# Kernel tuning notes

Hardware: AMD Instinct MI355X
Metric: run time of the kernel (lower is better)

Reference implementation:

```python
import jax, jax.numpy as jnp
import numpy as np

NUM_HEADS = 12
TOP_R = 0.1


def attention_rollout(attn_stack):
    # attn_stack: [L, B, H, N1, N1]; head_fusion='mean'
    A = attn_stack.mean(axis=2)                       # [L, B, N1, N1]
    n1 = A.shape[-1]
    A = A + jnp.eye(n1, dtype=A.dtype)                # residual connection
    A = A / A.sum(axis=-1, keepdims=True)             # row-normalize
    rollout = A[0]
    for l in range(1, A.shape[0]):                    # small fixed loop over layers
        rollout = A[l] @ rollout
    return rollout                                    # [B, N1, N1]


def setup_inputs() -> dict:
    key = jax.random.key(0)
    ks = jax.random.split(key, 7)
    B, N1, D, L, H = 32, 197, 768, 12, NUM_HEADS
    s = 1.0 / np.sqrt(D)
    return {
        "x": jax.random.normal(ks[0], (B, N1, D), dtype=jnp.float32),
        "attn_stack": jax.random.uniform(ks[1], (L, B, H, N1, N1), dtype=jnp.float32),
        "q_w": jax.random.normal(ks[2], (D, D), dtype=jnp.float32) * s,
        "k_w": jax.random.normal(ks[3], (D, D), dtype=jnp.float32) * s,
        "v_w": jax.random.normal(ks[4], (D, D), dtype=jnp.float32) * s,
        "proj_w": jax.random.normal(ks[5], (D, D), dtype=jnp.float32) * s,
        "proj_b": jnp.zeros((D,), dtype=jnp.float32),
    }


def reference(x, attn_stack, q_w, k_w, v_w, proj_w, proj_b):
    B, N1, C = x.shape
    N = N1 - 1
    H = NUM_HEADS
    hd = C // H
    scale = hd ** (-0.5)

    # --- attention rollout (detached in original) -> CLS attention over patches ---
    rollout = attention_rollout(jax.lax.stop_gradient(attn_stack))  # [B, N1, N1]
    cls_attention = rollout[:, 0, 1:]                               # [B, N]
    R = int(N * TOP_R)                                              # static top-R count
    _, top_indices = jax.lax.top_k(cls_attention, R)                # [B, R]

    # --- gather top-R local tokens (shift by 1 to skip CLS) ---
    x_local = jnp.take_along_axis(x, (top_indices + 1)[:, :, None], axis=1)  # [B, R, C]

    # --- projections ---
    q = (x_local @ q_w.T).reshape(B, R, H, hd).transpose(0, 2, 1, 3)   # [B, H, R, hd]
    k = (x @ k_w.T).reshape(B, N1, H, hd).transpose(0, 2, 1, 3)        # [B, H, N1, hd]
    v = (x @ v_w.T).reshape(B, N1, H, hd).transpose(0, 2, 1, 3)        # [B, H, N1, hd]

    # --- cross attention: local queries vs global key/values ---
    attn = jnp.einsum('bhrd,bhnd->bhrn', q, k) * scale                 # [B, H, R, N1]
    attn = jax.nn.softmax(attn, axis=-1)
    out = jnp.einsum('bhrn,bhnd->bhrd', attn, v)                       # [B, H, R, hd]
    out = out.transpose(0, 2, 1, 3).reshape(B, R, C)

    # --- output projection ---
    out = out @ proj_w.T + proj_b
    return out
```

## Files before the change

kernel.cpp:

```cpp
#include <hip/hip_runtime.h>
#include <math.h>

#define L_  12
#define B_  32
#define H_  12
#define N1_ 197
#define D_  768
#define R_  19
#define M_TOK (B_ * N1_)
#define NN (N1_ * N1_)

#define K1_FULL_ROWS  69344
#define K1_ROWS       69376
#define K1_BLOCKS     (K1_ROWS / 4)
#define PACK_ROWS     (M_TOK + 2304)
#define PACK_BLOCKS   ((PACK_ROWS * 12 + 255) / 256)
#define QKV_TILES     630

typedef __attribute__((ext_vector_type(8))) _Float16 f16x8;
typedef __attribute__((ext_vector_type(4))) float f32x4;

__device__ __forceinline__ f32x4 ld4u(const float* p) {
  f32x4 r; __builtin_memcpy(&r, p, 16); return r;
}
__device__ __forceinline__ void st4u(float* p, f32x4 v) {
  __builtin_memcpy(p, &v, 16);
}

__device__ __forceinline__ ushort f2h_bits(float f) {
  _Float16 h = (_Float16)f;
  ushort u; __builtin_memcpy(&u, &h, 2); return u;
}

typedef const __attribute__((address_space(1))) void* as1_vp;
typedef __attribute__((address_space(3))) void* as3_vp;
__device__ __forceinline__ void gl_lds16(const void* g, void* s) {
  __builtin_amdgcn_global_load_lds((as1_vp)g, (as3_vp)s, 16, 0, 0);
}

__global__ __launch_bounds__(256) void mega_k1_pack(const float* __restrict__ attn,
                                                    float* __restrict__ P,
                                                    float* __restrict__ dvec,
                                                    const float* __restrict__ x,
                                                    const float* __restrict__ k_w,
                                                    const float* __restrict__ v_w,
                                                    const float* __restrict__ q_w,
                                                    ushort* __restrict__ xpack,
                                                    ushort* __restrict__ wpack) {
  int bid = blockIdx.x;
  if (bid < K1_BLOCKS) {
    int wid = threadIdx.x >> 6;
    int t   = threadIdx.x & 63;
    int row_id = bid * 4 + wid;
    int l, b, i;
    if (row_id < K1_FULL_ROWS) {
      l = row_id / 6304;
      int rem = row_id - l * 6304;
      b = rem / 197;
      i = rem - b * 197;
    } else {
      l = 11; b = row_id - K1_FULL_ROWS; i = 0;
    }
    int lb   = l * B_ + b;
    int prow = lb * N1_ + i;
    const float* base = attn + (size_t)lb * (H_ * NN) + (size_t)i * N1_;
    f32x4 acc = {0.f, 0.f, 0.f, 0.f};
    if (t < 49) {
      const float* p = base + 4 * t;
#pragma unroll
      for (int h = 0; h < H_; ++h) acc += ld4u(p + (size_t)h * NN);
    } else if (t == 49) {
      const float* p = base + 196;
#pragma unroll
      for (int h = 0; h < H_; ++h) acc.x += p[(size_t)h * NN];
    }
    float s = (acc.x + acc.y) + (acc.z + acc.w);
#pragma unroll
    for (int o = 32; o; o >>= 1) s += __shfl_xor(s, o);
    float inv = 1.f / (s + 12.f);
    float* Pr = P + (size_t)prow * N1_;
    if (t < 49)       st4u(Pr + 4 * t, acc * inv);
    else if (t == 49) Pr[196] = acc.x * inv;
    if (t == 0) dvec[prow] = 12.f * inv;
  } else {
    int t = (bid - K1_BLOCKS) * 256 + threadIdx.x;
    if (t >= PACK_ROWS * 12) return;
    int row = t / 12, kb = t - row * 12;
    const float* src;
    ushort* dst;
    if (row < M_TOK) {
      src = x + (size_t)row * D_;
      dst = xpack + (size_t)row * 768;
    } else {
      int wr = row - M_TOK;
      int g = wr / 768, rl = wr - g * 768;
      const float* wsrc = (g == 0) ? k_w : (g == 1) ? v_w : q_w;
      src = wsrc + (size_t)rl * D_;
      dst = wpack + (size_t)wr * 768;
    }
    src += kb * 64;
    dst += kb * 64;
#pragma unroll
    for (int u = 0; u < 8; ++u) {
      float4 f = *(const float4*)(src + u * 8);
      float4 g = *(const float4*)(src + u * 8 + 4);
      f16x8 h;
      h[0] = (_Float16)f.x; h[1] = (_Float16)f.y;
      h[2] = (_Float16)f.z; h[3] = (_Float16)f.w;
      h[4] = (_Float16)g.x; h[5] = (_Float16)g.y;
      h[6] = (_Float16)g.z; h[7] = (_Float16)g.w;
      *(f16x8*)(dst + u * 8) = h;
    }
  }
}

__global__ __launch_bounds__(1024) void k2_chain_topk(const float* __restrict__ P,
                                                      const float* __restrict__ dvec,
                                                      int* __restrict__ gidx) {
  int b = blockIdx.x;
  __shared__ float v[N1_];
  __shared__ float part[4][N1_];
  int t = threadIdx.x, quar = t >> 8, j = t & 255;

  if (t < N1_) {
    const float* Pr = P + ((size_t)(11 * B_ + b) * N1_) * N1_;
    v[t] = Pr[t] + (t == 0 ? dvec[(11 * B_ + b) * N1_] : 0.f);
  }
  __syncthreads();

  for (int l = 10; l >= 0; --l) {
    if (j < N1_) {
      const float* Pc = P + ((size_t)(l * B_ + b) * N1_) * N1_ + j;
      float a[8] = {0.f, 0.f, 0.f, 0.f, 0.f, 0.f, 0.f, 0.f};
      int ibeg = (quar * N1_) / 4;
      int iend = ((quar + 1) * N1_) / 4;
      int i = ibeg;
      for (; i + 8 <= iend; i += 8) {
#pragma unroll
        for (int u = 0; u < 8; ++u)
          a[u] += v[i + u] * Pc[(size_t)(i + u) * N1_];
      }
      for (; i < iend; ++i) a[0] += v[i] * Pc[(size_t)i * N1_];
      float s = ((a[0] + a[1]) + (a[2] + a[3])) + ((a[4] + a[5]) + (a[6] + a[7]));
      if (quar == 0) s += v[j] * dvec[(l * B_ + b) * N1_ + j];
      part[quar][j] = s;
    }
    __syncthreads();
    if (t < N1_) v[t] = (part[0][t] + part[1][t]) + (part[2][t] + part[3][t]);
    __syncthreads();
  }

  if (t < 64) {
    float val[4];
    int   idx[4];
#pragma unroll
    for (int c = 0; c < 4; ++c) {
      int n = t + c * 64;
      bool ok = (n < N1_ - 1);
      val[c] = ok ? v[n + 1] : -1e30f;
      idx[c] = ok ? n : (1 << 20);
    }
    for (int r = 0; r < R_; ++r) {
      float bv = val[0];
      int   bi = idx[0];
#pragma unroll
      for (int c = 1; c < 4; ++c)
        if (val[c] > bv || (val[c] == bv && idx[c] < bi)) { bv = val[c]; bi = idx[c]; }
#pragma unroll
      for (int o = 32; o; o >>= 1) {
        float ov = __shfl_xor(bv, o);
        int   oi = __shfl_xor(bi, o);
        if (ov > bv || (ov == bv && oi < bi)) { bv = ov; bi = oi; }
      }
      if (t == 0) gidx[b * R_ + r] = b * N1_ + bi + 1;
#pragma unroll
      for (int c = 0; c < 4; ++c)
        if (idx[c] == bi) val[c] = -1e30f;
    }
  }
}

__global__ __launch_bounds__(256) void gemm_kvq_fast(const ushort* __restrict__ xpack,
                                                     const ushort* __restrict__ wpack,
                                                     const int* __restrict__ gidx,
                                                     float* __restrict__ kvb,
                                                     float* __restrict__ qbuf) {
  __shared__ __attribute__((aligned(16))) ushort As[128 * 64];
  __shared__ __attribute__((aligned(16))) ushort Bs[128 * 64];
  int tid = threadIdx.x, lane = tid & 63, wid = tid >> 6;
  int wr = wid >> 1, wc = wid & 1;
  int lr = lane & 15, lk = lane >> 4;

  int bid = blockIdx.x;
  int bm, wrow0, ccol0, ldc, Mrows;
  float* C;
  bool gath;
  if (bid < 600) {
    bm = bid % 50; int bn = bid / 50;
    wrow0 = bn * 128; ccol0 = bn * 128; ldc = 1536; Mrows = M_TOK;
    C = kvb; gath = false;
  } else {
    int tq = bid - 600;
    bm = tq % 5; int bn = tq / 5;
    wrow0 = 1536 + bn * 128; ccol0 = bn * 128; ldc = 768; Mrows = 608;
    C = qbuf; gath = true;
  }

  const ushort* asrc[4];
  const ushort* bsrc[4];
  ushort* adst[4];
  ushort* bdst[4];
  int lrow = lane >> 3, cpr = lane & 7;
#pragma unroll
  for (int i = 0; i < 4; ++i) {
    int r_loc = wid * 32 + i * 8 + lrow;
    int c     = cpr ^ (r_loc & 7);
    int ga    = bm * 128 + r_loc; if (ga >= Mrows) ga = Mrows - 1;
    int arow  = gath ? gidx[ga] : ga;
    asrc[i] = xpack + (size_t)arow * 768 + c * 8;
    bsrc[i] = wpack + (size_t)(wrow0 + r_loc) * 768 + c * 8;
    adst[i] = &As[(wid * 32 + i * 8) * 64];
    bdst[i] = &Bs[(wid * 32 + i * 8) * 64];
  }

  int o0 = (lk ^ (lr & 7)) * 8;
  int o1 = o0 ^ 32;

  f32x4 acc[4][4] = {};

#pragma unroll
  for (int i = 0; i < 4; ++i) { gl_lds16(asrc[i], adst[i]); gl_lds16(bsrc[i], bdst[i]); }

  for (int kb = 0; kb < 12; ++kb) {
    __syncthreads();
    f16x8 af0[4], af1[4], bf0[4], bf1[4];
#pragma unroll
    for (int m = 0; m < 4; ++m) {
      const ushort* rp = &As[(wr * 64 + m * 16 + lr) * 64];
      af0[m] = *(const f16x8*)(rp + o0);
      af1[m] = *(const f16x8*)(rp + o1);
    }
#pragma unroll
    for (int n = 0; n < 4; ++n) {
      const ushort* rp = &Bs[(wc * 64 + n * 16 + lr) * 64];
      bf0[n] = *(const f16x8*)(rp + o0);
      bf1[n] = *(const f16x8*)(rp + o1);
    }
    __syncthreads();
    if (kb < 11) {
#pragma unroll
      for (int i = 0; i < 4; ++i) {
        gl_lds16(asrc[i] + (kb + 1) * 64, adst[i]);
        gl_lds16(bsrc[i] + (kb + 1) * 64, bdst[i]);
      }
    }
#pragma unroll
    for (int m = 0; m < 4; ++m)
#pragma unroll
      for (int n = 0; n < 4; ++n) {
        acc[m][n] = __builtin_amdgcn_mfma_f32_16x16x32_f16(af0[m], bf0[n], acc[m][n], 0, 0, 0);
        acc[m][n] = __builtin_amdgcn_mfma_f32_16x16x32_f16(af1[m], bf1[n], acc[m][n], 0, 0, 0);
      }
  }

#pragma unroll
  for (int m = 0; m < 4; ++m) {
    int row0 = bm * 128 + wr * 64 + m * 16 + (lane >> 4) * 4;
#pragma unroll
    for (int i = 0; i < 4; ++i) {
      int row = row0 + i;
      if (row < Mrows) {
#pragma unroll
        for (int n = 0; n < 4; ++n) {
          int col = ccol0 + wc * 64 + n * 16 + lr;
          C[(size_t)row * ldc + col] = acc[m][n][i];
        }
      }
    }
  }
}

__global__ __launch_bounds__(256) void k5_attn(const float* __restrict__ kvb,
                                               const float* __restrict__ qb,
                                               float* __restrict__ ctx) {
  int bh = blockIdx.x;
  int b = bh / H_, h = bh % H_;
  __shared__ float ks[N1_][68];
  __shared__ float qs[R_][64];
  __shared__ float sc[R_][200];
  __shared__ float rsum[R_];
  int t = threadIdx.x;
  int lane = t & 63, wid = t >> 6;

  const float* kbase = kvb + (size_t)b * N1_ * 1536 + h * 64;
  for (int n = wid; n < N1_; n += 4)
    ks[n][lane] = kbase[(size_t)n * 1536 + lane];
  const float* qrow = qb + (size_t)b * R_ * D_ + h * 64;
  for (int e = t; e < R_ * 64; e += 256) {
    int r = e >> 6, d = e & 63;
    qs[r][d] = qrow[(size_t)r * D_ + d];
  }
  __syncthreads();

  if (t < N1_) {
    float accr[R_];
#pragma unroll
    for (int r = 0; r < R_; ++r) accr[r] = 0.f;
#pragma unroll
    for (int d0 = 0; d0 < 4; ++d0) {
      float4 k0 = *(const float4*)&ks[t][d0 * 16 + 0];
      float4 k1 = *(const float4*)&ks[t][d0 * 16 + 4];
      float4 k2 = *(const float4*)&ks[t][d0 * 16 + 8];
      float4 k3 = *(const float4*)&ks[t][d0 * 16 + 12];
#pragma unroll
      for (int r = 0; r < R_; ++r) {
        float4 q0 = *(const float4*)&qs[r][d0 * 16 + 0];
        float4 q1 = *(const float4*)&qs[r][d0 * 16 + 4];
        float4 q2 = *(const float4*)&qs[r][d0 * 16 + 8];
        float4 q3 = *(const float4*)&qs[r][d0 * 16 + 12];
        accr[r] += k0.x * q0.x + k0.y * q0.y + k0.z * q0.z + k0.w * q0.w
                 + k1.x * q1.x + k1.y * q1.y + k1.z * q1.z + k1.w * q1.w
                 + k2.x * q2.x + k2.y * q2.y + k2.z * q2.z + k2.w * q2.w
                 + k3.x * q3.x + k3.y * q3.y + k3.z * q3.z + k3.w * q3.w;
      }
    }
#pragma unroll
    for (int r = 0; r < R_; ++r) sc[r][t] = accr[r] * 0.125f;
  }
  __syncthreads();

  for (int r = wid; r < R_; r += 4) {
    float x0 = sc[r][lane];
    float x1 = sc[r][lane + 64];
    float x2 = sc[r][lane + 128];
    bool ok3 = (lane + 192 < N1_);
    float x3 = ok3 ? sc[r][lane + 192] : -1e30f;
    float m = fmaxf(fmaxf(x0, x1), fmaxf(x2, x3));
#pragma unroll
    for (int o = 32; o; o >>= 1) m = fmaxf(m, __shfl_xor(m, o));
    float e0 = expf(x0 - m), e1 = expf(x1 - m), e2 = expf(x2 - m);
    float e3 = ok3 ? expf(x3 - m) : 0.f;
    float s = e0 + e1 + e2 + e3;
#pragma unroll
    for (int o = 32; o; o >>= 1) s += __shfl_xor(s, o);
    sc[r][lane] = e0; sc[r][lane + 64] = e1; sc[r][lane + 128] = e2;
    if (ok3) sc[r][lane + 192] = e3;
    if (lane == 0) rsum[r] = s;
  }
  __syncthreads();

  const float* vb = kvb + (size_t)b * N1_ * 1536 + 768 + h * 64 + lane;
  int r0 = wid, r1 = wid + 4, r2 = wid + 8, r3 = wid + 12, r4 = wid + 16;
  bool has4 = (r4 < R_);
  float a0 = 0.f, a1 = 0.f, a2 = 0.f, a3 = 0.f, a4 = 0.f;
#pragma unroll 4
  for (int n = 0; n < N1_; ++n) {
    float vv = vb[(size_t)n * 1536];
    a0 += sc[r0][n] * vv;
    a1 += sc[r1][n] * vv;
    a2 += sc[r2][n] * vv;
    a3 += sc[r3][n] * vv;
    if (has4) a4 += sc[r4][n] * vv;
  }
  float* cb = ctx + (size_t)(b * R_) * D_ + h * 64 + lane;
  cb[(size_t)r0 * D_] = a0 / rsum[r0];
  cb[(size_t)r1 * D_] = a1 / rsum[r1];
  cb[(size_t)r2 * D_] = a2 / rsum[r2];
  cb[(size_t)r3 * D_] = a3 / rsum[r3];
  if (has4) cb[(size_t)r4 * D_] = a4 / rsum[r4];
}

#define PK 40
template <int BM, int BN, int MF, int NF>
__global__ __launch_bounds__(256) void gemm_f32in(const float* __restrict__ A,
                                                  const float* __restrict__ W0,
                                                  const float* __restrict__ bias,
                                                  float* __restrict__ C,
                                                  int M, int K, int ldc) {
  __shared__ __attribute__((aligned(16))) ushort As[BM][PK];
  __shared__ __attribute__((aligned(16))) ushort Bs[BN][PK];
  constexpr int TPRA = 256 / BM;
  constexpr int EPTA = 32 / TPRA;
  constexpr int NA4  = EPTA / 4;
  constexpr int TPRB = 256 / BN;
  constexpr int EPTB = 32 / TPRB;
  constexpr int NB4  = EPTB / 4;

  int tid  = threadIdx.x;
  int lane = tid & 63, wid = tid >> 6;
  int wr = wid >> 1, wc = wid & 1;
  int lr = lane & 15, lk = lane >> 4;
  int bm = blockIdx.x, bn = blockIdx.y;

  int arow_s = tid / TPRA;
  int akoff  = (tid % TPRA) * EPTA;
  int ar = bm * BM + arow_s; if (ar >= M) ar = M - 1;
  const float* ap = A + (size_t)ar * K + akoff;

  int brow_s = tid / TPRB;
  int bkoff  = (tid % TPRB) * EPTB;
  int wrow   = bn * BN + brow_s;
  const float* wp = W0 + (size_t)wrow * K + bkoff;

  f32x4 acc[MF][NF] = {};

  float4 pa[NA4], pb[NB4];
#pragma unroll
  for (int u = 0; u < NA4; ++u) pa[u] = *(const float4*)(ap + u * 4);
#pragma unroll
  for (int u = 0; u < NB4; ++u) pb[u] = *(const float4*)(wp + u * 4);

  for (int k0 = 0; k0 < K; k0 += 32) {
#pragma unroll
    for (int u = 0; u < NA4; ++u) {
      ushort4 h;
      h.x = f2h_bits(pa[u].x);
      h.y = f2h_bits(pa[u].y);
      h.z = f2h_bits(pa[u].z);
      h.w = f2h_bits(pa[u].w);
      *(ushort4*)&As[arow_s][akoff + u * 4] = h;
    }
#pragma unroll
    for (int u = 0; u < NB4; ++u) {
      ushort4 h;
      h.x = f2h_bits(pb[u].x);
      h.y = f2h_bits(pb[u].y);
      h.z = f2h_bits(pb[u].z);
      h.w = f2h_bits(pb[u].w);
      *(ushort4*)&Bs[brow_s][bkoff + u * 4] = h;
    }
    __syncthreads();

    int kn = k0 + 32;
    if (kn < K) {
#pragma unroll
      for (int u = 0; u < NA4; ++u) pa[u] = *(const float4*)(ap + kn + u * 4);
#pragma unroll
      for (int u = 0; u < NB4; ++u) pb[u] = *(const float4*)(wp + kn + u * 4);
    }

    f16x8 af[MF], bf[NF];
#pragma unroll
    for (int m = 0; m < MF; ++m)
      af[m] = *(const f16x8*)&As[wr * (BM / 2) + m * 16 + lr][lk * 8];
#pragma unroll
    for (int n = 0; n < NF; ++n)
      bf[n] = *(const f16x8*)&Bs[wc * (BN / 2) + n * 16 + lr][lk * 8];
#pragma unroll
    for (int m = 0; m < MF; ++m)
#pragma unroll
      for (int n = 0; n < NF; ++n)
        acc[m][n] = __builtin_amdgcn_mfma_f32_16x16x32_f16(af[m], bf[n], acc[m][n], 0, 0, 0);
    __syncthreads();
  }

#pragma unroll
  for (int m = 0; m < MF; ++m) {
    int row0 = bm * BM + wr * (BM / 2) + m * 16 + lk * 4;
#pragma unroll
    for (int i = 0; i < 4; ++i) {
      int row = row0 + i;
      if (row < M) {
#pragma unroll
        for (int n = 0; n < NF; ++n) {
          int col = bn * BN + wc * (BN / 2) + n * 16 + lr;
          float vv = acc[m][n][i];
          if (bias) vv += bias[col];
          C[(size_t)row * ldc + col] = vv;
        }
      }
    }
  }
}

extern "C" void kernel_launch(void* const* d_in, const int* in_sizes, int n_in,
                              void* d_out, int out_size, void* d_ws, size_t ws_size,
                              hipStream_t stream) {
  const float* x      = (const float*)d_in[0];
  const float* attn   = (const float*)d_in[1];
  const float* q_w    = (const float*)d_in[2];
  const float* k_w    = (const float*)d_in[3];
  const float* v_w    = (const float*)d_in[4];
  const float* proj_w = (const float*)d_in[5];
  const float* proj_b = (const float*)d_in[6];
  float* out = (float*)d_out;

  char* w = (char*)d_ws;
  auto take = [&](size_t bytes) { char* p = w; w += (bytes + 255) & ~(size_t)255; return p; };
  float*  P     = (float*)take((size_t)L_ * B_ * N1_ * N1_ * 4);
  float*  dvec  = (float*)take((size_t)L_ * B_ * N1_ * 4);
  int*    gidx  = (int*)take(B_ * R_ * 4);
  float*  kvb   = (float*)take((size_t)M_TOK * 1536 * 4);
  float*  qbuf  = (float*)take((size_t)B_ * R_ * D_ * 4);
  float*  ctx   = (float*)take((size_t)B_ * R_ * D_ * 4);
  ushort* xpack = (ushort*)take((size_t)M_TOK * 768 * 2);
  ushort* wpack = (ushort*)take((size_t)2304 * 768 * 2);

  hipLaunchKernelGGL(mega_k1_pack, dim3(K1_BLOCKS + PACK_BLOCKS), dim3(256), 0,
                     stream, attn, P, dvec, x, k_w, v_w, q_w, xpack, wpack);
  hipLaunchKernelGGL(k2_chain_topk, dim3(B_), dim3(1024), 0, stream, P, dvec, gidx);
  hipLaunchKernelGGL(gemm_kvq_fast, dim3(QKV_TILES), dim3(256), 0, stream,
                     xpack, wpack, gidx, kvb, qbuf);
  hipLaunchKernelGGL(k5_attn, dim3(B_ * H_), dim3(256), 0, stream, kvb, qbuf, ctx);
  hipLaunchKernelGGL((gemm_f32in<64, 64, 2, 2>), dim3(10, 12), dim3(256), 0, stream,
                     ctx, proj_w, proj_b, out, B_ * R_, D_, D_);
}
```

Baseline: 312.3 us.

## Compute Q for all tokens and overlap QKV GEMM with head-mean reduction

The QKV GEMM no longer waits for top-k. It now projects Q for every token rather than only the gathered ones, and runs in the same launch as the attention head-mean/normalize pass so the MFMA work overlaps the bandwidth-bound reduction. Packing to fp16 becomes its own kernel, and the attention kernel gathers Q rows by index from a unified qkv buffer. The rollout chain kernel also prefetches the next layer's column slice into registers to hide load latency. The trade-off is about 50% more GEMM FLOPs plus a larger intermediate buffer, and the chain kernel uses heavy per-thread register arrays.

```diff
diff --git a/kernel.cpp b/kernel.cpp
--- a/kernel.cpp
+++ b/kernel.cpp
@@ -15,7 +15,8 @@
 #define K1_BLOCKS     (K1_ROWS / 4)
 #define PACK_ROWS     (M_TOK + 2304)
 #define PACK_BLOCKS   ((PACK_ROWS * 12 + 255) / 256)
-#define QKV_TILES     630
+#define QKV_TILES     900
+#define MEGA_BLOCKS   (QKV_TILES + K1_BLOCKS)
 
 typedef __attribute__((ext_vector_type(8))) _Float16 f16x8;
 typedef __attribute__((ext_vector_type(4))) float f32x4;
@@ -25,11 +26,6 @@
 }
 __device__ __forceinline__ void st4u(float* p, f32x4 v) {
   __builtin_memcpy(p, &v, 16);
-}
-
-__device__ __forceinline__ ushort f2h_bits(float f) {
-  _Float16 h = (_Float16)f;
-  ushort u; __builtin_memcpy(&u, &h, 2); return u;
 }
 
 typedef const __attribute__((address_space(1))) void* as1_vp;
@@ -38,20 +34,132 @@
   __builtin_amdgcn_global_load_lds((as1_vp)g, (as3_vp)s, 16, 0, 0);
 }
 
-__global__ __launch_bounds__(256) void mega_k1_pack(const float* __restrict__ attn,
+__global__ __launch_bounds__(256) void pack_fp16(const float* __restrict__ x,
+                                                 const float* __restrict__ k_w,
+                                                 const float* __restrict__ v_w,
+                                                 const float* __restrict__ q_w,
+                                                 ushort* __restrict__ xpack,
+                                                 ushort* __restrict__ wpack) {
+  int t = blockIdx.x * 256 + threadIdx.x;
+  if (t >= PACK_ROWS * 12) return;
+  int row = t / 12, kb = t - row * 12;
+  const float* src;
+  ushort* dst;
+  if (row < M_TOK) {
+    src = x + (size_t)row * D_;
+    dst = xpack + (size_t)row * 768;
+  } else {
+    int wr = row - M_TOK;
+    int g = wr / 768, rl = wr - g * 768;
+    const float* wsrc = (g == 0) ? k_w : (g == 1) ? v_w : q_w;
+    src = wsrc + (size_t)rl * D_;
+    dst = wpack + (size_t)wr * 768;
+  }
+  src += kb * 64;
+  dst += kb * 64;
+#pragma unroll
+  for (int u = 0; u < 8; ++u) {
+    float4 f = *(const float4*)(src + u * 8);
+    float4 g = *(const float4*)(src + u * 8 + 4);
+    f16x8 h;
+    h[0] = (_Float16)f.x; h[1] = (_Float16)f.y;
+    h[2] = (_Float16)f.z; h[3] = (_Float16)f.w;
+    h[4] = (_Float16)g.x; h[5] = (_Float16)g.y;
+    h[6] = (_Float16)g.z; h[7] = (_Float16)g.w;
+    *(f16x8*)(dst + u * 8) = h;
+  }
+}
+
+__global__ __launch_bounds__(256) void mega_gemm_k1(const ushort* __restrict__ xpack,
+                                                    const ushort* __restrict__ wpack,
+                                                    float* __restrict__ qkv,
+                                                    const float* __restrict__ attn,
                                                     float* __restrict__ P,
-                                                    float* __restrict__ dvec,
-                                                    const float* __restrict__ x,
-                                                    const float* __restrict__ k_w,
-                                                    const float* __restrict__ v_w,
-                                                    const float* __restrict__ q_w,
-                                                    ushort* __restrict__ xpack,
-                                                    ushort* __restrict__ wpack) {
+                                                    float* __restrict__ dvec) {
+  __shared__ __attribute__((aligned(16))) ushort As[128 * 64];
+  __shared__ __attribute__((aligned(16))) ushort Bs[128 * 64];
   int bid = blockIdx.x;
-  if (bid < K1_BLOCKS) {
+  if (bid < QKV_TILES) {
+    int tid = threadIdx.x, lane = tid & 63, wid = tid >> 6;
+    int wr = wid >> 1, wc = wid & 1;
+    int lr = lane & 15, lk = lane >> 4;
+    int bm = bid % 50, bn = bid / 50;
+
+    const ushort* asrc[4];
+    const ushort* bsrc[4];
+    ushort* adst[4];
+    ushort* bdst[4];
+    int lrow = lane >> 3, cpr = lane & 7;
+#pragma unroll
+    for (int i = 0; i < 4; ++i) {
+      int r_loc = wid * 32 + i * 8 + lrow;
+      int c     = cpr ^ (r_loc & 7);
+      int ga    = bm * 128 + r_loc; if (ga >= M_TOK) ga = M_TOK - 1;
+      asrc[i] = xpack + (size_t)ga * 768 + c * 8;
+      bsrc[i] = wpack + (size_t)(bn * 128 + r_loc) * 768 + c * 8;
+      adst[i] = &As[(wid * 32 + i * 8) * 64];
+      bdst[i] = &Bs[(wid * 32 + i * 8) * 64];
+    }
+
+    int o0 = (lk ^ (lr & 7)) * 8;
+    int o1 = o0 ^ 32;
+
+    f32x4 acc[4][4] = {};
+
+#pragma unroll
+    for (int i = 0; i < 4; ++i) { gl_lds16(asrc[i], adst[i]); gl_lds16(bsrc[i], bdst[i]); }
+
+    for (int kb = 0; kb < 12; ++kb) {
+      __syncthreads();
+      f16x8 af0[4], af1[4], bf0[4], bf1[4];
+#pragma unroll
+      for (int m = 0; m < 4; ++m) {
+        const ushort* rp = &As[(wr * 64 + m * 16 + lr) * 64];
+        af0[m] = *(const f16x8*)(rp + o0);
+        af1[m] = *(const f16x8*)(rp + o1);
+      }
+#pragma unroll
+      for (int n = 0; n < 4; ++n) {
+        const ushort* rp = &Bs[(wc * 64 + n * 16 + lr) * 64];
+        bf0[n] = *(const f16x8*)(rp + o0);
+        bf1[n] = *(const f16x8*)(rp + o1);
+      }
+      __syncthreads();
+      if (kb < 11) {
+#pragma unroll
+        for (int i = 0; i < 4; ++i) {
+          gl_lds16(asrc[i] + (kb + 1) * 64, adst[i]);
+          gl_lds16(bsrc[i] + (kb + 1) * 64, bdst[i]);
+        }
+      }
+#pragma unroll
+      for (int m = 0; m < 4; ++m)
+#pragma unroll
+        for (int n = 0; n < 4; ++n) {
+          acc[m][n] = __builtin_amdgcn_mfma_f32_16x16x32_f16(af0[m], bf0[n], acc[m][n], 0, 0, 0);
+          acc[m][n] = __builtin_amdgcn_mfma_f32_16x16x32_f16(af1[m], bf1[n], acc[m][n], 0, 0, 0);
+        }
+    }
+
+#pragma unroll
+    for (int m = 0; m < 4; ++m) {
+      int row0 = bm * 128 + wr * 64 + m * 16 + (lane >> 4) * 4;
+#pragma unroll
+      for (int i = 0; i < 4; ++i) {
+        int row = row0 + i;
+        if (row < M_TOK) {
+#pragma unroll
+          for (int n = 0; n < 4; ++n) {
+            int col = bn * 128 + wc * 64 + n * 16 + lr;
+            qkv[(size_t)row * 2304 + col] = acc[m][n][i];
+          }
+        }
+      }
+    }
+  } else {
     int wid = threadIdx.x >> 6;
     int t   = threadIdx.x & 63;
-    int row_id = bid * 4 + wid;
+    int row_id = (bid - QKV_TILES) * 4 + wid;
     int l, b, i;
     if (row_id < K1_FULL_ROWS) {
       l = row_id / 6304;
@@ -82,35 +190,6 @@
     if (t < 49)       st4u(Pr + 4 * t, acc * inv);
     else if (t == 49) Pr[196] = acc.x * inv;
     if (t == 0) dvec[prow] = 12.f * inv;
-  } else {
-    int t = (bid - K1_BLOCKS) * 256 + threadIdx.x;
-    if (t >= PACK_ROWS * 12) return;
-    int row = t / 12, kb = t - row * 12;
-    const float* src;
-    ushort* dst;
-    if (row < M_TOK) {
-      src = x + (size_t)row * D_;
-      dst = xpack + (size_t)row * 768;
-    } else {
-      int wr = row - M_TOK;
-      int g = wr / 768, rl = wr - g * 768;
-      const float* wsrc = (g == 0) ? k_w : (g == 1) ? v_w : q_w;
-      src = wsrc + (size_t)rl * D_;
-      dst = wpack + (size_t)wr * 768;
-    }
-    src += kb * 64;
-    dst += kb * 64;
-#pragma unroll
-    for (int u = 0; u < 8; ++u) {
-      float4 f = *(const float4*)(src + u * 8);
-      float4 g = *(const float4*)(src + u * 8 + 4);
-      f16x8 h;
-      h[0] = (_Float16)f.x; h[1] = (_Float16)f.y;
-      h[2] = (_Float16)f.z; h[3] = (_Float16)f.w;
-      h[4] = (_Float16)g.x; h[5] = (_Float16)g.y;
-      h[6] = (_Float16)g.z; h[7] = (_Float16)g.w;
-      *(f16x8*)(dst + u * 8) = h;
-    }
   }
 }
 
@@ -121,33 +200,54 @@
   __shared__ float v[N1_];
   __shared__ float part[4][N1_];
   int t = threadIdx.x, quar = t >> 8, j = t & 255;
+  int ibeg = (quar * N1_) / 4;
+  bool last50 = (quar == 3);
 
   if (t < N1_) {
     const float* Pr = P + ((size_t)(11 * B_ + b) * N1_) * N1_;
     v[t] = Pr[t] + (t == 0 ? dvec[(11 * B_ + b) * N1_] : 0.f);
   }
+
+  float cur[50], nxt[50];
+  if (j < N1_) {
+    const float* Pc = P + ((size_t)(10 * B_ + b) * N1_) * N1_ + j;
+#pragma unroll
+    for (int u = 0; u < 50; ++u) {
+      int i = ibeg + u; if (i > 196) i = 196;
+      cur[u] = Pc[(size_t)i * N1_];
+    }
+  }
   __syncthreads();
 
   for (int l = 10; l >= 0; --l) {
+    if (l > 0 && j < N1_) {
+      const float* Pc = P + ((size_t)((l - 1) * B_ + b) * N1_) * N1_ + j;
+#pragma unroll
+      for (int u = 0; u < 50; ++u) {
+        int i = ibeg + u; if (i > 196) i = 196;
+        nxt[u] = Pc[(size_t)i * N1_];
+      }
+    }
     if (j < N1_) {
-      const float* Pc = P + ((size_t)(l * B_ + b) * N1_) * N1_ + j;
-      float a[8] = {0.f, 0.f, 0.f, 0.f, 0.f, 0.f, 0.f, 0.f};
-      int ibeg = (quar * N1_) / 4;
-      int iend = ((quar + 1) * N1_) / 4;
-      int i = ibeg;
-      for (; i + 8 <= iend; i += 8) {
-#pragma unroll
-        for (int u = 0; u < 8; ++u)
-          a[u] += v[i + u] * Pc[(size_t)(i + u) * N1_];
-      }
-      for (; i < iend; ++i) a[0] += v[i] * Pc[(size_t)i * N1_];
-      float s = ((a[0] + a[1]) + (a[2] + a[3])) + ((a[4] + a[5]) + (a[6] + a[7]));
+      float a0 = 0.f, a1 = 0.f, a2 = 0.f, a3 = 0.f;
+#pragma unroll
+      for (int u = 0; u < 48; u += 4) {
+        a0 += v[ibeg + u]     * cur[u];
+        a1 += v[ibeg + u + 1] * cur[u + 1];
+        a2 += v[ibeg + u + 2] * cur[u + 2];
+        a3 += v[ibeg + u + 3] * cur[u + 3];
+      }
+      a0 += v[ibeg + 48] * cur[48];
+      if (last50) a1 += v[ibeg + 49] * cur[49];
+      float s = (a0 + a1) + (a2 + a3);
       if (quar == 0) s += v[j] * dvec[(l * B_ + b) * N1_ + j];
       part[quar][j] = s;
     }
     __syncthreads();
     if (t < N1_) v[t] = (part[0][t] + part[1][t]) + (part[2][t] + part[3][t]);
     __syncthreads();
+#pragma unroll
+    for (int u = 0; u < 50; ++u) cur[u] = nxt[u];
   }
 
   if (t < 64) {
@@ -180,108 +280,8 @@
   }
 }
 
-__global__ __launch_bounds__(256) void gemm_kvq_fast(const ushort* __restrict__ xpack,
-                                                     const ushort* __restrict__ wpack,
-                                                     const int* __restrict__ gidx,
-                                                     float* __restrict__ kvb,
-                                                     float* __restrict__ qbuf) {
-  __shared__ __attribute__((aligned(16))) ushort As[128 * 64];
-  __shared__ __attribute__((aligned(16))) ushort Bs[128 * 64];
-  int tid = threadIdx.x, lane = tid & 63, wid = tid >> 6;
-  int wr = wid >> 1, wc = wid & 1;
-  int lr = lane & 15, lk = lane >> 4;
-
-  int bid = blockIdx.x;
-  int bm, wrow0, ccol0, ldc, Mrows;
-  float* C;
-  bool gath;
-  if (bid < 600) {
-    bm = bid % 50; int bn = bid / 50;
-    wrow0 = bn * 128; ccol0 = bn * 128; ldc = 1536; Mrows = M_TOK;
-    C = kvb; gath = false;
-  } else {
-    int tq = bid - 600;
-    bm = tq % 5; int bn = tq / 5;
-    wrow0 = 1536 + bn * 128; ccol0 = bn * 128; ldc = 768; Mrows = 608;
-    C = qbuf; gath = true;
-  }
-
-  const ushort* asrc[4];
-  const ushort* bsrc[4];
-  ushort* adst[4];
-  ushort* bdst[4];
-  int lrow = lane >> 3, cpr = lane & 7;
-#pragma unroll
-  for (int i = 0; i < 4; ++i) {
-    int r_loc = wid * 32 + i * 8 + lrow;
-    int c     = cpr ^ (r_loc & 7);
-    int ga    = bm * 128 + r_loc; if (ga >= Mrows) ga = Mrows - 1;
-    int arow  = gath ? gidx[ga] : ga;
-    asrc[i] = xpack + (size_t)arow * 768 + c * 8;
-    bsrc[i] = wpack + (size_t)(wrow0 + r_loc) * 768 + c * 8;
-    adst[i] = &As[(wid * 32 + i * 8) * 64];
-    bdst[i] = &Bs[(wid * 32 + i * 8) * 64];
-  }
-
-  int o0 = (lk ^ (lr & 7)) * 8;
-  int o1 = o0 ^ 32;
-
-  f32x4 acc[4][4] = {};
-
-#pragma unroll
-  for (int i = 0; i < 4; ++i) { gl_lds16(asrc[i], adst[i]); gl_lds16(bsrc[i], bdst[i]); }
-
-  for (int kb = 0; kb < 12; ++kb) {
-    __syncthreads();
-    f16x8 af0[4], af1[4], bf0[4], bf1[4];
-#pragma unroll
-    for (int m = 0; m < 4; ++m) {
-      const ushort* rp = &As[(wr * 64 + m * 16 + lr) * 64];
-      af0[m] = *(const f16x8*)(rp + o0);
-      af1[m] = *(const f16x8*)(rp + o1);
-    }
-#pragma unroll
-    for (int n = 0; n < 4; ++n) {
-      const ushort* rp = &Bs[(wc * 64 + n * 16 + lr) * 64];
-      bf0[n] = *(const f16x8*)(rp + o0);
-      bf1[n] = *(const f16x8*)(rp + o1);
-    }
-    __syncthreads();
-    if (kb < 11) {
-#pragma unroll
-      for (int i = 0; i < 4; ++i) {
-        gl_lds16(asrc[i] + (kb + 1) * 64, adst[i]);
-        gl_lds16(bsrc[i] + (kb + 1) * 64, bdst[i]);
-      }
-    }
-#pragma unroll
-    for (int m = 0; m < 4; ++m)
-#pragma unroll
-      for (int n = 0; n < 4; ++n) {
-        acc[m][n] = __builtin_amdgcn_mfma_f32_16x16x32_f16(af0[m], bf0[n], acc[m][n], 0, 0, 0);
-        acc[m][n] = __builtin_amdgcn_mfma_f32_16x16x32_f16(af1[m], bf1[n], acc[m][n], 0, 0, 0);
-      }
-  }
-
-#pragma unroll
-  for (int m = 0; m < 4; ++m) {
-    int row0 = bm * 128 + wr * 64 + m * 16 + (lane >> 4) * 4;
-#pragma unroll
-    for (int i = 0; i < 4; ++i) {
-      int row = row0 + i;
-      if (row < Mrows) {
-#pragma unroll
-        for (int n = 0; n < 4; ++n) {
-          int col = ccol0 + wc * 64 + n * 16 + lr;
-          C[(size_t)row * ldc + col] = acc[m][n][i];
-        }
-      }
-    }
-  }
-}
-
-__global__ __launch_bounds__(256) void k5_attn(const float* __restrict__ kvb,
-                                               const float* __restrict__ qb,
+__global__ __launch_bounds__(256) void k5_attn(const float* __restrict__ qkv,
+                                               const int* __restrict__ gidx,
                                                float* __restrict__ ctx) {
   int bh = blockIdx.x;
   int b = bh / H_, h = bh % H_;
@@ -292,13 +292,13 @@
   int t = threadIdx.x;
   int lane = t & 63, wid = t >> 6;
 
-  const float* kbase = kvb + (size_t)b * N1_ * 1536 + h * 64;
+  const float* kbase = qkv + (size_t)(b * N1_) * 2304 + h * 64;
   for (int n = wid; n < N1_; n += 4)
-    ks[n][lane] = kbase[(size_t)n * 1536 + lane];
-  const float* qrow = qb + (size_t)b * R_ * D_ + h * 64;
+    ks[n][lane] = kbase[(size_t)n * 2304 + lane];
   for (int e = t; e < R_ * 64; e += 256) {
     int r = e >> 6, d = e & 63;
-    qs[r][d] = qrow[(size_t)r * D_ + d];
+    int grow = gidx[b * R_ + r];
+    qs[r][d] = qkv[(size_t)grow * 2304 + 1536 + h * 64 + d];
   }
   __syncthreads();
 
@@ -349,13 +349,13 @@
   }
   __syncthreads();
 
-  const float* vb = kvb + (size_t)b * N1_ * 1536 + 768 + h * 64 + lane;
+  const float* vb = qkv + (size_t)(b * N1_) * 2304 + 768 + h * 64 + lane;
   int r0 = wid, r1 = wid + 4, r2 = wid + 8, r3 = wid + 12, r4 = wid + 16;
   bool has4 = (r4 < R_);
   float a0 = 0.f, a1 = 0.f, a2 = 0.f, a3 = 0.f, a4 = 0.f;
 #pragma unroll 4
   for (int n = 0; n < N1_; ++n) {
-    float vv = vb[(size_t)n * 1536];
+    float vv = vb[(size_t)n * 2304];
     a0 += sc[r0][n] * vv;
     a1 += sc[r1][n] * vv;
     a2 += sc[r2][n] * vv;
@@ -368,6 +368,11 @@
   cb[(size_t)r2 * D_] = a2 / rsum[r2];
   cb[(size_t)r3 * D_] = a3 / rsum[r3];
   if (has4) cb[(size_t)r4 * D_] = a4 / rsum[r4];
+}
+
+__device__ __forceinline__ ushort f2h_bits(float f) {
+  _Float16 h = (_Float16)f;
+  ushort u; __builtin_memcpy(&u, &h, 2); return u;
 }
 
 #define PK 40
@@ -490,18 +495,17 @@
   float*  P     = (float*)take((size_t)L_ * B_ * N1_ * N1_ * 4);
   float*  dvec  = (float*)take((size_t)L_ * B_ * N1_ * 4);
   int*    gidx  = (int*)take(B_ * R_ * 4);
-  float*  kvb   = (float*)take((size_t)M_TOK * 1536 * 4);
-  float*  qbuf  = (float*)take((size_t)B_ * R_ * D_ * 4);
+  float*  qkv   = (float*)take((size_t)M_TOK * 2304 * 4);
   float*  ctx   = (float*)take((size_t)B_ * R_ * D_ * 4);
   ushort* xpack = (ushort*)take((size_t)M_TOK * 768 * 2);
   ushort* wpack = (ushort*)take((size_t)2304 * 768 * 2);
 
-  hipLaunchKernelGGL(mega_k1_pack, dim3(K1_BLOCKS + PACK_BLOCKS), dim3(256), 0,
-                     stream, attn, P, dvec, x, k_w, v_w, q_w, xpack, wpack);
+  hipLaunchKernelGGL(pack_fp16, dim3(PACK_BLOCKS), dim3(256), 0, stream,
+                     x, k_w, v_w, q_w, xpack, wpack);
+  hipLaunchKernelGGL(mega_gemm_k1, dim3(MEGA_BLOCKS), dim3(256), 0, stream,
+                     xpack, wpack, qkv, attn, P, dvec);
   hipLaunchKernelGGL(k2_chain_topk, dim3(B_), dim3(1024), 0, stream, P, dvec, gidx);
-  hipLaunchKernelGGL(gemm_kvq_fast, dim3(QKV_TILES), dim3(256), 0, stream,
-                     xpack, wpack, gidx, kvb, qbuf);
-  hipLaunchKernelGGL(k5_attn, dim3(B_ * H_), dim3(256), 0, stream, kvb, qbuf, ctx);
+  hipLaunchKernelGGL(k5_attn, dim3(B_ * H_), dim3(256), 0, stream, qkv, gidx, ctx);
   hipLaunchKernelGGL((gemm_f32in<64, 64, 2, 2>), dim3(10, 12), dim3(256), 0, stream,
                      ctx, proj_w, proj_b, out, B_ * R_, D_, D_);
 }
```

After: 359.8 us. 15.2% more time.

## Store K/V/Q in fp16, stage V in LDS, prefetch rollout chain rows

Applied to the files above, without the earlier changes.

The QKV GEMM now writes K, V and Q intermediates as fp16 rather than fp32, which halves that buffer's write traffic and the attention kernel's read traffic. The attention kernel converts V into shared memory once instead of reading it from global memory with a large stride inside the inner loop. The rollout chain kernel prefetches the next layer's matrix column into registers while the current layer is computed, to hide load latency in the serial chain. Risks are extra fp16 rounding error on K/V/Q and higher register pressure from the 100 float prefetch arrays in the 1024-thread kernel, which could cause spills.

```diff
diff --git a/kernel.cpp b/kernel.cpp
--- a/kernel.cpp
+++ b/kernel.cpp
@@ -26,10 +26,12 @@
 __device__ __forceinline__ void st4u(float* p, f32x4 v) {
   __builtin_memcpy(p, &v, 16);
 }
-
 __device__ __forceinline__ ushort f2h_bits(float f) {
   _Float16 h = (_Float16)f;
   ushort u; __builtin_memcpy(&u, &h, 2); return u;
+}
+__device__ __forceinline__ float h2f(ushort u) {
+  _Float16 h; __builtin_memcpy(&h, &u, 2); return (float)h;
 }
 
 typedef const __attribute__((address_space(1))) void* as1_vp;
@@ -121,33 +123,54 @@
   __shared__ float v[N1_];
   __shared__ float part[4][N1_];
   int t = threadIdx.x, quar = t >> 8, j = t & 255;
+  int ibeg = (quar * N1_) / 4;
+  bool last50 = (quar == 3);
 
   if (t < N1_) {
     const float* Pr = P + ((size_t)(11 * B_ + b) * N1_) * N1_;
     v[t] = Pr[t] + (t == 0 ? dvec[(11 * B_ + b) * N1_] : 0.f);
   }
+
+  float cur[50], nxt[50];
+  if (j < N1_) {
+    const float* Pc = P + ((size_t)(10 * B_ + b) * N1_) * N1_ + j;
+#pragma unroll
+    for (int u = 0; u < 50; ++u) {
+      int i = ibeg + u; if (i > 196) i = 196;
+      cur[u] = Pc[(size_t)i * N1_];
+    }
+  }
   __syncthreads();
 
   for (int l = 10; l >= 0; --l) {
+    if (l > 0 && j < N1_) {
+      const float* Pc = P + ((size_t)((l - 1) * B_ + b) * N1_) * N1_ + j;
+#pragma unroll
+      for (int u = 0; u < 50; ++u) {
+        int i = ibeg + u; if (i > 196) i = 196;
+        nxt[u] = Pc[(size_t)i * N1_];
+      }
+    }
     if (j < N1_) {
-      const float* Pc = P + ((size_t)(l * B_ + b) * N1_) * N1_ + j;
-      float a[8] = {0.f, 0.f, 0.f, 0.f, 0.f, 0.f, 0.f, 0.f};
-      int ibeg = (quar * N1_) / 4;
-      int iend = ((quar + 1) * N1_) / 4;
-      int i = ibeg;
-      for (; i + 8 <= iend; i += 8) {
-#pragma unroll
-        for (int u = 0; u < 8; ++u)
-          a[u] += v[i + u] * Pc[(size_t)(i + u) * N1_];
-      }
-      for (; i < iend; ++i) a[0] += v[i] * Pc[(size_t)i * N1_];
-      float s = ((a[0] + a[1]) + (a[2] + a[3])) + ((a[4] + a[5]) + (a[6] + a[7]));
+      float a0 = 0.f, a1 = 0.f, a2 = 0.f, a3 = 0.f;
+#pragma unroll
+      for (int u = 0; u < 48; u += 4) {
+        a0 += v[ibeg + u]     * cur[u];
+        a1 += v[ibeg + u + 1] * cur[u + 1];
+        a2 += v[ibeg + u + 2] * cur[u + 2];
+        a3 += v[ibeg + u + 3] * cur[u + 3];
+      }
+      a0 += v[ibeg + 48] * cur[48];
+      if (last50) a1 += v[ibeg + 49] * cur[49];
+      float s = (a0 + a1) + (a2 + a3);
       if (quar == 0) s += v[j] * dvec[(l * B_ + b) * N1_ + j];
       part[quar][j] = s;
     }
     __syncthreads();
     if (t < N1_) v[t] = (part[0][t] + part[1][t]) + (part[2][t] + part[3][t]);
     __syncthreads();
+#pragma unroll
+    for (int u = 0; u < 50; ++u) cur[u] = nxt[u];
   }
 
   if (t < 64) {
@@ -183,8 +206,8 @@
 __global__ __launch_bounds__(256) void gemm_kvq_fast(const ushort* __restrict__ xpack,
                                                      const ushort* __restrict__ wpack,
                                                      const int* __restrict__ gidx,
-                                                     float* __restrict__ kvb,
-                                                     float* __restrict__ qbuf) {
+                                                     ushort* __restrict__ kvb,
+                                                     ushort* __restrict__ qbuf) {
   __shared__ __attribute__((aligned(16))) ushort As[128 * 64];
   __shared__ __attribute__((aligned(16))) ushort Bs[128 * 64];
   int tid = threadIdx.x, lane = tid & 63, wid = tid >> 6;
@@ -193,7 +216,7 @@
 
   int bid = blockIdx.x;
   int bm, wrow0, ccol0, ldc, Mrows;
-  float* C;
+  ushort* C;
   bool gath;
   if (bid < 600) {
     bm = bid % 50; int bn = bid / 50;
@@ -273,15 +296,15 @@
 #pragma unroll
         for (int n = 0; n < 4; ++n) {
           int col = ccol0 + wc * 64 + n * 16 + lr;
-          C[(size_t)row * ldc + col] = acc[m][n][i];
+          C[(size_t)row * ldc + col] = f2h_bits(acc[m][n][i]);
         }
       }
     }
   }
 }
 
-__global__ __launch_bounds__(256) void k5_attn(const float* __restrict__ kvb,
-                                               const float* __restrict__ qb,
+__global__ __launch_bounds__(256) void k5_attn(const ushort* __restrict__ kvb,
+                                               const ushort* __restrict__ qb,
                                                float* __restrict__ ctx) {
   int bh = blockIdx.x;
   int b = bh / H_, h = bh % H_;
@@ -292,13 +315,13 @@
   int t = threadIdx.x;
   int lane = t & 63, wid = t >> 6;
 
-  const float* kbase = kvb + (size_t)b * N1_ * 1536 + h * 64;
+  const ushort* kb16 = kvb + (size_t)b * N1_ * 1536 + h * 64;
   for (int n = wid; n < N1_; n += 4)
-    ks[n][lane] = kbase[(size_t)n * 1536 + lane];
-  const float* qrow = qb + (size_t)b * R_ * D_ + h * 64;
+    ks[n][lane] = h2f(kb16[(size_t)n * 1536 + lane]);
+  const ushort* qb16 = qb + (size_t)(b * R_) * 768 + h * 64;
   for (int e = t; e < R_ * 64; e += 256) {
     int r = e >> 6, d = e & 63;
-    qs[r][d] = qrow[(size_t)r * D_ + d];
+    qs[r][d] = h2f(qb16[(size_t)r * 768 + d]);
   }
   __syncthreads();
 
@@ -329,6 +352,10 @@
   }
   __syncthreads();
 
+  const ushort* vb16 = kvb + (size_t)b * N1_ * 1536 + 768 + h * 64;
+  for (int n = wid; n < N1_; n += 4)
+    ks[n][lane] = h2f(vb16[(size_t)n * 1536 + lane]);
+
   for (int r = wid; r < R_; r += 4) {
     float x0 = sc[r][lane];
     float x1 = sc[r][lane + 64];
@@ -349,13 +376,12 @@
   }
   __syncthreads();
 
-  const float* vb = kvb + (size_t)b * N1_ * 1536 + 768 + h * 64 + lane;
   int r0 = wid, r1 = wid + 4, r2 = wid + 8, r3 = wid + 12, r4 = wid + 16;
   bool has4 = (r4 < R_);
   float a0 = 0.f, a1 = 0.f, a2 = 0.f, a3 = 0.f, a4 = 0.f;
 #pragma unroll 4
   for (int n = 0; n < N1_; ++n) {
-    float vv = vb[(size_t)n * 1536];
+    float vv = ks[n][lane];
     a0 += sc[r0][n] * vv;
     a1 += sc[r1][n] * vv;
     a2 += sc[r2][n] * vv;
@@ -490,8 +516,8 @@
   float*  P     = (float*)take((size_t)L_ * B_ * N1_ * N1_ * 4);
   float*  dvec  = (float*)take((size_t)L_ * B_ * N1_ * 4);
   int*    gidx  = (int*)take(B_ * R_ * 4);
-  float*  kvb   = (float*)take((size_t)M_TOK * 1536 * 4);
-  float*  qbuf  = (float*)take((size_t)B_ * R_ * D_ * 4);
+  ushort* kvb   = (ushort*)take((size_t)M_TOK * 1536 * 2);
+  ushort* qbuf  = (ushort*)take((size_t)B_ * R_ * D_ * 2);
   float*  ctx   = (float*)take((size_t)B_ * R_ * D_ * 4);
   ushort* xpack = (ushort*)take((size_t)M_TOK * 768 * 2);
   ushort* wpack = (ushort*)take((size_t)2304 * 768 * 2);
```

After: 314.8 us (median of 2 runs). Within noise of the previous version (+0.8%).
